# Kernel optimization log

Hardware: AMD Instinct MI355X
Metric: run time of the kernel (lower is better)

## Reference

```python
import jax, jax.numpy as jnp
import numpy as np

B, M, F = 32, 32768, 256


def setup_inputs() -> dict:
    key = jax.random.key(0)
    ks = jax.random.split(key, 6)
    scale1 = 1.0 / np.sqrt(2 * F)
    scale2 = 1.0 / np.sqrt(F)
    return {
        "input_data": jax.random.normal(ks[0], (B, F), dtype=jnp.float32),
        "memory": jax.random.normal(ks[1], (M, F), dtype=jnp.float32),
        "W1": jax.random.uniform(ks[2], (F, 2 * F), jnp.float32, -scale1, scale1),
        "b1": jax.random.uniform(ks[3], (F,), jnp.float32, -scale1, scale1),
        "W2": jax.random.uniform(ks[4], (1, F), jnp.float32, -scale2, scale2),
        "b2": jax.random.uniform(ks[5], (1,), jnp.float32, -scale2, scale2),
        # threshold below 1/M so the conditional scatter-write path actually fires
        # (torch default 0.05 with random weights never writes for M=32768)
        "threshold": jnp.float32(1e-5),
    }


def reference(input_data, memory, W1, b1, W2, b2, threshold):
    # Linear on cat([x, mem]) splits into two independent matmuls.
    W1x, W1m = W1[:, :F], W1[:, F:]          # each [F, F]
    hx = input_data @ W1x.T                   # [B, F]
    hm = memory @ W1m.T                       # [M, F]
    h = jnp.tanh(hx[:, None, :] + hm[None, :, :] + b1)  # [B, M, F]
    scores = h @ W2[0] + b2[0]                # [B, M]
    weights = jax.nn.softmax(scores, axis=1)  # softmax over memory slots
    best = jnp.argmax(weights, axis=1)        # [B] winning slot per item
    maxw = jnp.max(weights, axis=1)           # [B]
    mask = maxw > threshold                   # write only if above threshold
    # Sequential loop semantics: later batch items overwrite earlier ones
    # at the same slot. last[s] = 1 + index of last masked writer to slot s.
    order = jnp.where(mask, jnp.arange(B, dtype=jnp.int32) + 1, 0)
    last = jax.ops.segment_max(order, best, num_segments=M)  # [M]
    last = jnp.maximum(last, 0)
    src = input_data[jnp.maximum(last - 1, 0)]               # [M, F]
    updated_memory = jnp.where((last > 0)[:, None], src, memory)
    return updated_memory
```

## Files before the change

### kernel.cpp

```cpp
#include <hip/hip_runtime.h>

#define FDIM 256
#define BDIM 32
#define MDIM 32768
#define NB   512

#define WS_EM    0
#define WS_EX    (WS_EM + MDIM*FDIM)
#define WS_W2N   (WS_EX + BDIM*FDIM)
#define WS_PMAX  (WS_W2N + FDIM)
#define WS_PSUM  (WS_PMAX + BDIM*NB)
#define WS_PARG  (WS_PSUM + BDIM*NB)
#define WS_WIN   (WS_PARG + BDIM*NB)
#define WS_BEST  (WS_WIN + 32)
#define WS_GMAX  (WS_BEST + 32)
#define WS_GSUM  (WS_GMAX + 32)
#define WS_GARG  (WS_GSUM + 32)
#define WS_WH    (WS_GARG + 32)
#define WS_WL    (WS_WH + 32768)

#define C2 2.8853900817779268f

typedef __attribute__((ext_vector_type(8))) short bf16x8;
typedef __attribute__((ext_vector_type(8))) unsigned short ushort8;
typedef __attribute__((ext_vector_type(4))) unsigned short ushort4v;
typedef __attribute__((ext_vector_type(4))) float f32x4;

__device__ inline unsigned short f2bf(float x) {
  unsigned u = __float_as_uint(x);
  return (unsigned short)((u + 0x7fffu + ((u >> 16) & 1u)) >> 16);
}
__device__ inline float bf2f(unsigned short h) {
  return __uint_as_float(((unsigned)h) << 16);
}

__global__ __launch_bounds__(256) void k1_prep(const float* __restrict__ input,
                                               const float* __restrict__ W1,
                                               const float* __restrict__ b1,
                                               const float* __restrict__ W2,
                                               float* __restrict__ Ex,
                                               float* __restrict__ w2n,
                                               unsigned short* __restrict__ wh,
                                               unsigned short* __restrict__ wl) {
  if (blockIdx.x < BDIM) {
    const int b = blockIdx.x, f = threadIdx.x;
    const float* in = input + b * FDIM;
    const float* w  = W1 + (size_t)f * 512;
    float acc = b1[f];
    #pragma unroll 8
    for (int k = 0; k < FDIM; k += 4) {
      float4 iv = *(const float4*)(in + k);
      float4 wv = *(const float4*)(w + k);
      acc = fmaf(iv.x, wv.x, acc); acc = fmaf(iv.y, wv.y, acc);
      acc = fmaf(iv.z, wv.z, acc); acc = fmaf(iv.w, wv.w, acc);
    }
    Ex[b * FDIM + f] = __builtin_amdgcn_exp2f(acc * C2);
    if (b == 0) w2n[f] = -2.0f * W2[f];
  } else {
    int id = ((blockIdx.x - BDIM) * 256 + threadIdx.x) * 4;
    int f = id >> 8, c = id & 255;
    float4 v = *(const float4*)(W1 + (size_t)f * 512 + 256 + c);
    float xs[4] = {v.x, v.y, v.z, v.w};
    #pragma unroll
    for (int e = 0; e < 4; ++e) {
      unsigned short h = f2bf(xs[e]);
      wh[id + e] = h;
      wl[id + e] = f2bf(xs[e] - bf2f(h));
    }
  }
}

__global__ __launch_bounds__(1024, 8) void k23_fused(const float* __restrict__ mem,
                                                     const unsigned short* __restrict__ wh,
                                                     const unsigned short* __restrict__ wl,
                                                     const float* __restrict__ Ex,
                                                     const float* __restrict__ w2n,
                                                     float* __restrict__ pmax,
                                                     float* __restrict__ psum,
                                                     int* __restrict__ parg,
                                                     float* __restrict__ out) {
  __shared__ __align__(16) char smem[51200];
  unsigned short* AH = (unsigned short*)(smem);
  unsigned short* AL = (unsigned short*)(smem + 5120);
  unsigned short* BH = (unsigned short*)(smem + 10240);
  unsigned short* BL = (unsigned short*)(smem + 30720);
  float* emT = (float*)smem;

  const int tid = threadIdx.x;
  const int lane = tid & 63, wid = tid >> 6;
  const int m0 = blockIdx.x * 64;
  const int rb = lane & 15, g8 = (lane >> 4) * 8;
  const int mh = wid & 3;
  const int fq = wid >> 2;

  f32x4 acc[4];
  #pragma unroll
  for (int j = 0; j < 4; ++j) acc[j] = (f32x4){0.f, 0.f, 0.f, 0.f};

  for (int s = 0; s < 8; ++s) {
    const int k0 = s * 32;
    __syncthreads();
    if (tid < 512) {
      int r = tid >> 3, c4 = (tid & 7) * 4;
      const float* mrow = mem + (size_t)(m0 + r) * 256 + k0 + c4;
      float4 a0 = *(const float4*)(mrow);
      *(float4*)(out + (size_t)(m0 + r) * 256 + k0 + c4) = a0;
      float xs[4] = {a0.x, a0.y, a0.z, a0.w};
      ushort4v ahv, alv;
      #pragma unroll
      for (int e = 0; e < 4; ++e) {
        unsigned short h = f2bf(xs[e]);
        ahv[e] = h;
        alv[e] = f2bf(xs[e] - bf2f(h));
      }
      *(ushort4v*)&AH[r * 40 + c4] = ahv;
      *(ushort4v*)&AL[r * 40 + c4] = alv;
    } else {
      int t2 = tid - 512;
      #pragma unroll
      for (int q = 0; q < 2; ++q) {
        int id = q * 512 + t2, br = id >> 2, bc = (id & 3) * 8;
        *(uint4*)&BH[br * 40 + bc] = *(const uint4*)(wh + (size_t)br * 256 + k0 + bc);
        *(uint4*)&BL[br * 40 + bc] = *(const uint4*)(wl + (size_t)br * 256 + k0 + bc);
      }
    }
    __syncthreads();

    bf16x8 fah, fal, fbh[4], fbl[4];
    fah = *(const bf16x8*)&AH[(mh * 16 + rb) * 40 + g8];
    fal = *(const bf16x8*)&AL[(mh * 16 + rb) * 40 + g8];
    #pragma unroll
    for (int j = 0; j < 4; ++j) {
      fbh[j] = *(const bf16x8*)&BH[(fq * 64 + j * 16 + rb) * 40 + g8];
      fbl[j] = *(const bf16x8*)&BL[(fq * 64 + j * 16 + rb) * 40 + g8];
    }
    #pragma unroll
    for (int j = 0; j < 4; ++j) {
      acc[j] = __builtin_amdgcn_mfma_f32_16x16x32_bf16(fah, fbh[j], acc[j], 0, 0, 0);
      acc[j] = __builtin_amdgcn_mfma_f32_16x16x32_bf16(fah, fbl[j], acc[j], 0, 0, 0);
      acc[j] = __builtin_amdgcn_mfma_f32_16x16x32_bf16(fal, fbh[j], acc[j], 0, 0, 0);
    }
  }

  const int wuid = __builtin_amdgcn_readfirstlane(wid);
  const float* ex0 = Ex + (size_t)(wuid * 2 + 0) * FDIM;
  const float* ex1 = Ex + (size_t)(wuid * 2 + 1) * FDIM;
  float acc0 = 0.f, acc1 = 0.f;

  #pragma unroll
  for (int h = 0; h < 2; ++h) {
    __syncthreads();
    if ((wid >> 3) == h) {
      #pragma unroll
      for (int j = 0; j < 4; ++j) {
        const int fl = (fq * 64 + j * 16 + rb) - h * 128;
        const int mloc = mh * 16 + (lane >> 4) * 4;
        float4 v;
        v.x = __builtin_amdgcn_exp2f(acc[j][0] * C2);
        v.y = __builtin_amdgcn_exp2f(acc[j][1] * C2);
        v.z = __builtin_amdgcn_exp2f(acc[j][2] * C2);
        v.w = __builtin_amdgcn_exp2f(acc[j][3] * C2);
        *(float4*)(emT + fl * 68 + mloc) = v;
      }
    }
    __syncthreads();

    #pragma unroll 2
    for (int fl2 = 0; fl2 < 128; fl2 += 4) {
      const int fg = h * 128 + fl2;
      float e0 = emT[(fl2 + 0) * 68 + lane];
      float e1 = emT[(fl2 + 1) * 68 + lane];
      float e2 = emT[(fl2 + 2) * 68 + lane];
      float e3 = emT[(fl2 + 3) * 68 + lane];
      float w0 = w2n[fg + 0], w1 = w2n[fg + 1];
      float w2 = w2n[fg + 2], w3 = w2n[fg + 3];
      #define SCORE4(exP, accV)                                          \
      {                                                                  \
        float u0 = fmaf(e0, exP[fg + 0], 1.f);                           \
        float u1 = fmaf(e1, exP[fg + 1], 1.f);                           \
        float u2 = fmaf(e2, exP[fg + 2], 1.f);                           \
        float u3 = fmaf(e3, exP[fg + 3], 1.f);                           \
        float p01 = u0 * u1, p23 = u2 * u3;                              \
        float den = p01 * p23;                                           \
        float t0 = fmaf(w1, u0, w0 * u1);                                \
        float t1 = fmaf(w3, u2, w2 * u3);                                \
        float num = fmaf(t1, p01, t0 * p23);                             \
        accV = fmaf(num, __builtin_amdgcn_rcpf(den), accV);              \
      }
      SCORE4(ex0, acc0)
      SCORE4(ex1, acc1)
      #undef SCORE4
    }
  }

  float accb[2] = {acc0, acc1};
  const int blk = blockIdx.x;
  #pragma unroll
  for (int bi = 0; bi < 2; ++bi) {
    float s = accb[bi]; int idx = m0 + lane;
    #pragma unroll
    for (int off = 32; off > 0; off >>= 1) {
      float so = __shfl_xor(s, off);
      int   io = __shfl_xor(idx, off);
      if (so > s || (so == s && io < idx)) { s = so; idx = io; }
    }
    float ex = __expf(accb[bi] - s);
    #pragma unroll
    for (int off = 32; off > 0; off >>= 1) ex += __shfl_xor(ex, off);
    if (lane == 0) {
      int b = wuid * 2 + bi;
      pmax[b * NB + blk] = s;
      psum[b * NB + blk] = ex;
      parg[b * NB + blk] = idx;
    }
  }
}

__global__ __launch_bounds__(1024) void k45_finish(const float* __restrict__ pmax,
                                                   const float* __restrict__ psum,
                                                   const int* __restrict__ parg,
                                                   const float* __restrict__ thr_p,
                                                   const float* __restrict__ input,
                                                   float* __restrict__ out) {
  __shared__ float gm[BDIM], gs[BDIM];
  __shared__ int   ga[BDIM], wn[BDIM];
  const int tid = threadIdx.x, lane = tid & 63, w = tid >> 6;
  #pragma unroll
  for (int half = 0; half < 2; ++half) {
    const int b = w * 2 + half;
    float cm = -3.0e38f, cs = 0.f; int ca = 0x7fffffff;
    #pragma unroll
    for (int t = 0; t < NB / 64; ++t) {
      int i = t * 64 + lane;
      float s = pmax[b * NB + i];
      float p = psum[b * NB + i];
      int   a = parg[b * NB + i];
      if (s > cm)      { cs = cs * __expf(cm - s) + p; cm = s; ca = a; }
      else if (s == cm){ cs += p; if (a < ca) ca = a; }
      else             { cs += p * __expf(s - cm); }
    }
    #pragma unroll
    for (int off = 32; off > 0; off >>= 1) {
      float om = __shfl_xor(cm, off);
      float os = __shfl_xor(cs, off);
      int   oa = __shfl_xor(ca, off);
      if (om > cm)      { cs = cs * __expf(cm - om) + os; cm = om; ca = oa; }
      else if (om == cm){ cs += os; if (oa < ca) ca = oa; }
      else              { cs += os * __expf(om - cm); }
    }
    if (lane == 0) { gm[b] = cm; gs[b] = cs; ga[b] = ca; }
  }
  __syncthreads();
  if (tid < BDIM) {
    const float thr = *thr_p;
    const int me = ga[tid];
    int w_ = (1.0f / gs[tid] > thr) ? 1 : 0;
    if (w_) {
      for (int b2 = tid + 1; b2 < BDIM; ++b2)
        if ((1.0f / gs[b2] > thr) && ga[b2] == me) { w_ = 0; break; }
    }
    wn[tid] = w_;
  }
  __syncthreads();
  {
    const int b = tid >> 5, sub = tid & 31;
    if (wn[b]) {
      const int m = ga[b];
      *(float4*)(out + (size_t)m * 256 + sub * 8) =
          *(const float4*)(input + (size_t)b * 256 + sub * 8);
      *(float4*)(out + (size_t)m * 256 + sub * 8 + 4) =
          *(const float4*)(input + (size_t)b * 256 + sub * 8 + 4);
    }
  }
}

extern "C" void kernel_launch(void* const* d_in, const int* in_sizes, int n_in,
                              void* d_out, int out_size, void* d_ws, size_t ws_size,
                              hipStream_t stream) {
  const float* input  = (const float*)d_in[0];
  const float* memory = (const float*)d_in[1];
  const float* W1     = (const float*)d_in[2];
  const float* b1     = (const float*)d_in[3];
  const float* W2     = (const float*)d_in[4];
  const float* thr    = (const float*)d_in[6];

  float* ws   = (float*)d_ws;
  float* Ex   = ws + WS_EX;
  float* w2n  = ws + WS_W2N;
  float* pmax = ws + WS_PMAX;
  float* psum = ws + WS_PSUM;
  int*   parg = (int*)(ws + WS_PARG);
  unsigned short* wh = (unsigned short*)(ws + WS_WH);
  unsigned short* wl = (unsigned short*)(ws + WS_WL);
  float* out  = (float*)d_out;

  hipLaunchKernelGGL(k1_prep,    dim3(BDIM + 64), dim3(256),  0, stream, input, W1, b1, W2, Ex, w2n, wh, wl);
  hipLaunchKernelGGL(k23_fused,  dim3(MDIM / 64), dim3(1024), 0, stream, memory, wh, wl, Ex, w2n, pmax, psum, parg, out);
  hipLaunchKernelGGL(k45_finish, dim3(1),         dim3(1024), 0, stream, pmax, psum, parg, thr, input, out);
}
```

Before: 72.85 us.

## Double-buffer LDS stages in fused GEMM loop to overlap loads with MFMA

The K-loop of the fused kernel now uses two LDS buffers. Each stage's global loads and bf16 split are issued into one buffer while MFMA runs on the other, which halves the barriers per step. This roughly doubles shared memory per block to 100 KB and relaxes the launch-bounds occupancy hint, so fewer blocks may be resident per CU. The gain depends on whether the extra overlap outweighs that occupancy loss.

```diff
diff --git a/kernel.cpp b/kernel.cpp
--- a/kernel.cpp
+++ b/kernel.cpp
@@ -70,7 +70,7 @@
   }
 }
 
-__global__ __launch_bounds__(1024, 8) void k23_fused(const float* __restrict__ mem,
+__global__ __launch_bounds__(1024, 4) void k23_fused(const float* __restrict__ mem,
                                                      const unsigned short* __restrict__ wh,
                                                      const unsigned short* __restrict__ wl,
                                                      const float* __restrict__ Ex,
@@ -79,11 +79,11 @@
                                                      float* __restrict__ psum,
                                                      int* __restrict__ parg,
                                                      float* __restrict__ out) {
-  __shared__ __align__(16) char smem[51200];
-  unsigned short* AH = (unsigned short*)(smem);
-  unsigned short* AL = (unsigned short*)(smem + 5120);
-  unsigned short* BH = (unsigned short*)(smem + 10240);
-  unsigned short* BL = (unsigned short*)(smem + 30720);
+  __shared__ __align__(16) char smem[102400];
+  unsigned short* AHp[2] = {(unsigned short*)(smem),         (unsigned short*)(smem + 51200)};
+  unsigned short* ALp[2] = {(unsigned short*)(smem + 5120),  (unsigned short*)(smem + 56320)};
+  unsigned short* BHp[2] = {(unsigned short*)(smem + 10240), (unsigned short*)(smem + 61440)};
+  unsigned short* BLp[2] = {(unsigned short*)(smem + 30720), (unsigned short*)(smem + 81920)};
   float* emT = (float*)smem;
 
   const int tid = threadIdx.x;
@@ -97,9 +97,8 @@
   #pragma unroll
   for (int j = 0; j < 4; ++j) acc[j] = (f32x4){0.f, 0.f, 0.f, 0.f};
 
-  for (int s = 0; s < 8; ++s) {
+  auto STAGE = [&](int s, int buf) {
     const int k0 = s * 32;
-    __syncthreads();
     if (tid < 512) {
       int r = tid >> 3, c4 = (tid & 7) * 4;
       const float* mrow = mem + (size_t)(m0 + r) * 256 + k0 + c4;
@@ -113,26 +112,27 @@
         ahv[e] = h;
         alv[e] = f2bf(xs[e] - bf2f(h));
       }
-      *(ushort4v*)&AH[r * 40 + c4] = ahv;
-      *(ushort4v*)&AL[r * 40 + c4] = alv;
+      *(ushort4v*)&AHp[buf][r * 40 + c4] = ahv;
+      *(ushort4v*)&ALp[buf][r * 40 + c4] = alv;
     } else {
       int t2 = tid - 512;
       #pragma unroll
       for (int q = 0; q < 2; ++q) {
         int id = q * 512 + t2, br = id >> 2, bc = (id & 3) * 8;
-        *(uint4*)&BH[br * 40 + bc] = *(const uint4*)(wh + (size_t)br * 256 + k0 + bc);
-        *(uint4*)&BL[br * 40 + bc] = *(const uint4*)(wl + (size_t)br * 256 + k0 + bc);
+        *(uint4*)&BHp[buf][br * 40 + bc] = *(const uint4*)(wh + (size_t)br * 256 + k0 + bc);
+        *(uint4*)&BLp[buf][br * 40 + bc] = *(const uint4*)(wl + (size_t)br * 256 + k0 + bc);
       }
     }
-    __syncthreads();
-
+  };
+
+  auto COMPUTE = [&](int buf) {
     bf16x8 fah, fal, fbh[4], fbl[4];
-    fah = *(const bf16x8*)&AH[(mh * 16 + rb) * 40 + g8];
-    fal = *(const bf16x8*)&AL[(mh * 16 + rb) * 40 + g8];
+    fah = *(const bf16x8*)&AHp[buf][(mh * 16 + rb) * 40 + g8];
+    fal = *(const bf16x8*)&ALp[buf][(mh * 16 + rb) * 40 + g8];
     #pragma unroll
     for (int j = 0; j < 4; ++j) {
-      fbh[j] = *(const bf16x8*)&BH[(fq * 64 + j * 16 + rb) * 40 + g8];
-      fbl[j] = *(const bf16x8*)&BL[(fq * 64 + j * 16 + rb) * 40 + g8];
+      fbh[j] = *(const bf16x8*)&BHp[buf][(fq * 64 + j * 16 + rb) * 40 + g8];
+      fbl[j] = *(const bf16x8*)&BLp[buf][(fq * 64 + j * 16 + rb) * 40 + g8];
     }
     #pragma unroll
     for (int j = 0; j < 4; ++j) {
@@ -140,6 +140,17 @@
       acc[j] = __builtin_amdgcn_mfma_f32_16x16x32_bf16(fah, fbl[j], acc[j], 0, 0, 0);
       acc[j] = __builtin_amdgcn_mfma_f32_16x16x32_bf16(fal, fbh[j], acc[j], 0, 0, 0);
     }
+  };
+
+  STAGE(0, 0);
+  #pragma unroll
+  for (int s2 = 0; s2 < 8; s2 += 2) {
+    __syncthreads();
+    if (s2 < 7) STAGE(s2 + 1, 1);
+    COMPUTE(0);
+    __syncthreads();
+    if (s2 + 2 < 8) STAGE(s2 + 2, 0);
+    COMPUTE(1);
   }
 
   const int wuid = __builtin_amdgcn_readfirstlane(wid);
```

New measurement: 83.91 us. +15.2%, slower.

## Fold finish kernel into main kernel via last-block ticket and transpose exp tile

Applied to the files above, without the earlier changes.

Removes the separate single-block finish launch by having each block of the fused kernel take an atomic ticket; the last block performs the global softmax/argmax merge and conditional writes. The exp tile in shared memory is stored m-major with padding 132 so the score loop reads a float4 per lane instead of four scalar loads. Launch bounds minimum blocks changes from 8 to 4, relaxing the register constraint. Adds a threadfence plus an atomic per block and a counter reset in the prep kernel.

```diff
diff --git a/kernel.cpp b/kernel.cpp
--- a/kernel.cpp
+++ b/kernel.cpp
@@ -11,18 +11,13 @@
 #define WS_PMAX  (WS_W2N + FDIM)
 #define WS_PSUM  (WS_PMAX + BDIM*NB)
 #define WS_PARG  (WS_PSUM + BDIM*NB)
-#define WS_WIN   (WS_PARG + BDIM*NB)
-#define WS_BEST  (WS_WIN + 32)
-#define WS_GMAX  (WS_BEST + 32)
-#define WS_GSUM  (WS_GMAX + 32)
-#define WS_GARG  (WS_GSUM + 32)
-#define WS_WH    (WS_GARG + 32)
+#define WS_CNT   (WS_PARG + BDIM*NB)
+#define WS_WH    (WS_CNT + 32)
 #define WS_WL    (WS_WH + 32768)
 
 #define C2 2.8853900817779268f
 
 typedef __attribute__((ext_vector_type(8))) short bf16x8;
-typedef __attribute__((ext_vector_type(8))) unsigned short ushort8;
 typedef __attribute__((ext_vector_type(4))) unsigned short ushort4v;
 typedef __attribute__((ext_vector_type(4))) float f32x4;
 
@@ -41,7 +36,9 @@
                                                float* __restrict__ Ex,
                                                float* __restrict__ w2n,
                                                unsigned short* __restrict__ wh,
-                                               unsigned short* __restrict__ wl) {
+                                               unsigned short* __restrict__ wl,
+                                               int* __restrict__ cnt) {
+  if (blockIdx.x == 0 && threadIdx.x == 0) cnt[0] = 0;
   if (blockIdx.x < BDIM) {
     const int b = blockIdx.x, f = threadIdx.x;
     const float* in = input + b * FDIM;
@@ -70,7 +67,7 @@
   }
 }
 
-__global__ __launch_bounds__(1024, 8) void k23_fused(const float* __restrict__ mem,
+__global__ __launch_bounds__(1024, 4) void k23_fused(const float* __restrict__ mem,
                                                      const unsigned short* __restrict__ wh,
                                                      const unsigned short* __restrict__ wl,
                                                      const float* __restrict__ Ex,
@@ -78,13 +75,18 @@
                                                      float* __restrict__ pmax,
                                                      float* __restrict__ psum,
                                                      int* __restrict__ parg,
+                                                     const float* __restrict__ thr_p,
+                                                     const float* __restrict__ input,
+                                                     int* __restrict__ cnt,
                                                      float* __restrict__ out) {
   __shared__ __align__(16) char smem[51200];
   unsigned short* AH = (unsigned short*)(smem);
   unsigned short* AL = (unsigned short*)(smem + 5120);
   unsigned short* BH = (unsigned short*)(smem + 10240);
   unsigned short* BL = (unsigned short*)(smem + 30720);
-  float* emT = (float*)smem;
+  float* emM = (float*)smem;
+  __shared__ float gm_s[BDIM], gs_s[BDIM];
+  __shared__ int   ga_s[BDIM], wn_s[BDIM], ticket_s;
 
   const int tid = threadIdx.x;
   const int lane = tid & 63, wid = tid >> 6;
@@ -151,16 +153,14 @@
   for (int h = 0; h < 2; ++h) {
     __syncthreads();
     if ((wid >> 3) == h) {
+      const int fbase = (fq - 2 * h) * 64 + rb;
+      const int mbase = mh * 16 + (lane >> 4) * 4;
       #pragma unroll
       for (int j = 0; j < 4; ++j) {
-        const int fl = (fq * 64 + j * 16 + rb) - h * 128;
-        const int mloc = mh * 16 + (lane >> 4) * 4;
-        float4 v;
-        v.x = __builtin_amdgcn_exp2f(acc[j][0] * C2);
-        v.y = __builtin_amdgcn_exp2f(acc[j][1] * C2);
-        v.z = __builtin_amdgcn_exp2f(acc[j][2] * C2);
-        v.w = __builtin_amdgcn_exp2f(acc[j][3] * C2);
-        *(float4*)(emT + fl * 68 + mloc) = v;
+        #pragma unroll
+        for (int r = 0; r < 4; ++r)
+          emM[(mbase + r) * 132 + fbase + j * 16] =
+              __builtin_amdgcn_exp2f(acc[j][r] * C2);
       }
     }
     __syncthreads();
@@ -168,10 +168,8 @@
     #pragma unroll 2
     for (int fl2 = 0; fl2 < 128; fl2 += 4) {
       const int fg = h * 128 + fl2;
-      float e0 = emT[(fl2 + 0) * 68 + lane];
-      float e1 = emT[(fl2 + 1) * 68 + lane];
-      float e2 = emT[(fl2 + 2) * 68 + lane];
-      float e3 = emT[(fl2 + 3) * 68 + lane];
+      float4 ev = *(const float4*)&emM[lane * 132 + fl2];
+      float e0 = ev.x, e1 = ev.y, e2 = ev.z, e3 = ev.w;
       float w0 = w2n[fg + 0], w1 = w2n[fg + 1];
       float w2 = w2n[fg + 2], w3 = w2n[fg + 3];
       #define SCORE4(exP, accV)                                          \
@@ -214,20 +212,16 @@
       parg[b * NB + blk] = idx;
     }
   }
-}
-
-__global__ __launch_bounds__(1024) void k45_finish(const float* __restrict__ pmax,
-                                                   const float* __restrict__ psum,
-                                                   const int* __restrict__ parg,
-                                                   const float* __restrict__ thr_p,
-                                                   const float* __restrict__ input,
-                                                   float* __restrict__ out) {
-  __shared__ float gm[BDIM], gs[BDIM];
-  __shared__ int   ga[BDIM], wn[BDIM];
-  const int tid = threadIdx.x, lane = tid & 63, w = tid >> 6;
+
+  __threadfence();
+  if (tid == 0) ticket_s = atomicAdd(cnt, 1);
+  __syncthreads();
+  if (ticket_s != (int)gridDim.x - 1) return;
+  __threadfence();
+
   #pragma unroll
   for (int half = 0; half < 2; ++half) {
-    const int b = w * 2 + half;
+    const int b = wid * 2 + half;
     float cm = -3.0e38f, cs = 0.f; int ca = 0x7fffffff;
     #pragma unroll
     for (int t = 0; t < NB / 64; ++t) {
@@ -248,24 +242,24 @@
       else if (om == cm){ cs += os; if (oa < ca) ca = oa; }
       else              { cs += os * __expf(om - cm); }
     }
-    if (lane == 0) { gm[b] = cm; gs[b] = cs; ga[b] = ca; }
+    if (lane == 0) { gm_s[b] = cm; gs_s[b] = cs; ga_s[b] = ca; }
   }
   __syncthreads();
   if (tid < BDIM) {
     const float thr = *thr_p;
-    const int me = ga[tid];
-    int w_ = (1.0f / gs[tid] > thr) ? 1 : 0;
+    const int me = ga_s[tid];
+    int w_ = (1.0f / gs_s[tid] > thr) ? 1 : 0;
     if (w_) {
       for (int b2 = tid + 1; b2 < BDIM; ++b2)
-        if ((1.0f / gs[b2] > thr) && ga[b2] == me) { w_ = 0; break; }
-    }
-    wn[tid] = w_;
+        if ((1.0f / gs_s[b2] > thr) && ga_s[b2] == me) { w_ = 0; break; }
+    }
+    wn_s[tid] = w_;
   }
   __syncthreads();
   {
     const int b = tid >> 5, sub = tid & 31;
-    if (wn[b]) {
-      const int m = ga[b];
+    if (wn_s[b]) {
+      const int m = ga_s[b];
       *(float4*)(out + (size_t)m * 256 + sub * 8) =
           *(const float4*)(input + (size_t)b * 256 + sub * 8);
       *(float4*)(out + (size_t)m * 256 + sub * 8 + 4) =
@@ -290,11 +284,11 @@
   float* pmax = ws + WS_PMAX;
   float* psum = ws + WS_PSUM;
   int*   parg = (int*)(ws + WS_PARG);
+  int*   cnt  = (int*)(ws + WS_CNT);
   unsigned short* wh = (unsigned short*)(ws + WS_WH);
   unsigned short* wl = (unsigned short*)(ws + WS_WL);
   float* out  = (float*)d_out;
 
-  hipLaunchKernelGGL(k1_prep,    dim3(BDIM + 64), dim3(256),  0, stream, input, W1, b1, W2, Ex, w2n, wh, wl);
-  hipLaunchKernelGGL(k23_fused,  dim3(MDIM / 64), dim3(1024), 0, stream, memory, wh, wl, Ex, w2n, pmax, psum, parg, out);
-  hipLaunchKernelGGL(k45_finish, dim3(1),         dim3(1024), 0, stream, pmax, psum, parg, thr, input, out);
-}
+  hipLaunchKernelGGL(k1_prep,   dim3(BDIM + 64), dim3(256),  0, stream, input, W1, b1, W2, Ex, w2n, wh, wl, cnt);
+  hipLaunchKernelGGL(k23_fused, dim3(MDIM / 64), dim3(1024), 0, stream, memory, wh, wl, Ex, w2n, pmax, psum, parg, thr, input, cnt, out);
+}
```

Measured after the change: 242.6 us. +233.1%, slower.
